# Performance work log

Hardware: AMD Instinct MI355X
Metric: run time of the kernel (lower is better)

## Reference

```python
import jax, jax.numpy as jnp
import numpy as np

DIM = 1024
HEADS = 16
DIM_HEAD = 64
DEPTH = 12
LN_EPS = 1e-5


def setup_inputs() -> dict:
    key = jax.random.key(0)
    k1, k2, k3 = jax.random.split(key, 3)
    B, N = 4, 2048
    inner = HEADS * DIM_HEAD
    x = jax.random.normal(k1, (B, N, DIM), dtype=jnp.float32)
    ln_w = jnp.ones((DIM,), jnp.float32)
    ln_b = jnp.zeros((DIM,), jnp.float32)
    w_qkv = jax.random.normal(k2, (DIM, 3 * inner), jnp.float32) * (DIM ** -0.5)
    w_out = jax.random.normal(k3, (inner, DIM), jnp.float32) * (inner ** -0.5)
    b_out = jnp.zeros((DIM,), jnp.float32)
    return {"x": x, "ln_w": ln_w, "ln_b": ln_b, "w_qkv": w_qkv,
            "w_out": w_out, "b_out": b_out, "layer_index": 2}


def reference(x, ln_w, ln_b, w_qkv, w_out, b_out, layer_index):
    B, N, D = x.shape
    scale = DIM_HEAD ** -0.5
    # LayerNorm
    mu = jnp.mean(x, axis=-1, keepdims=True)
    var = jnp.mean(jnp.square(x - mu), axis=-1, keepdims=True)
    xn = (x - mu) * jax.lax.rsqrt(var + LN_EPS) * ln_w + ln_b
    # QKV projection (no bias), split heads: b n (h d) -> b h n d
    qkv = xn @ w_qkv  # [B, N, 3*H*Dh]
    q, k, v = jnp.split(qkv, 3, axis=-1)
    def heads(t):
        return t.reshape(B, N, HEADS, DIM_HEAD).transpose(0, 2, 1, 3)
    q, k, v = heads(q), heads(k), heads(v)
    dots = jnp.einsum('bhnd,bhmd->bhnm', q, k) * scale  # [B,H,N,N]
    if layer_index < DEPTH // 2:
        attn = jax.nn.relu(dots)
    else:
        attn = jax.nn.softmax(dots, axis=-1)
    attn = attn / N  # divide by x.shape[1]
    out = jnp.einsum('bhnm,bhmd->bhnd', attn, v)
    out = out.transpose(0, 2, 1, 3).reshape(B, N, HEADS * DIM_HEAD)
    # to_out (heads > 1): Linear + (inactive) dropout
    return out @ w_out + b_out
```

## Files before the change

kernel.cpp:

```cpp
#include <hip/hip_runtime.h>
#include <stdint.h>

typedef __bf16 bf16x8 __attribute__((ext_vector_type(8)));
typedef __bf16 bf16x4 __attribute__((ext_vector_type(4)));
typedef float f32x4 __attribute__((ext_vector_type(4)));
typedef float f32x16 __attribute__((ext_vector_type(16)));

#define PSCALE (0.125f / 2048.0f)

#define GLOAD16(src, dst)                                                      \
  __builtin_amdgcn_global_load_lds(                                            \
      (__attribute__((address_space(1))) void*)const_cast<__bf16*>(src),       \
      (__attribute__((address_space(3))) void*)(dst), 16, 0, 0)

__global__ __launch_bounds__(256) void prep(
    const float* __restrict__ x, const float* __restrict__ lw,
    const float* __restrict__ lb, __bf16* __restrict__ xn,
    const float* __restrict__ w_qkv, __bf16* __restrict__ Wt1,
    const float* __restrict__ w_out, __bf16* __restrict__ Wt2) {
  __shared__ __bf16 T[64][72];
  __shared__ float red[8];
  const int b = blockIdx.x;
  const int t = threadIdx.x;
  if (b < 8192) {
    const float4 v = ((const float4*)(x + (size_t)b * 1024))[t];
    float s = v.x + v.y + v.z + v.w;
    float ss = v.x * v.x + v.y * v.y + v.z * v.z + v.w * v.w;
#pragma unroll
    for (int o = 32; o; o >>= 1) {
      s += __shfl_down(s, o);
      ss += __shfl_down(ss, o);
    }
    if ((t & 63) == 0) {
      red[t >> 6] = s;
      red[4 + (t >> 6)] = ss;
    }
    __syncthreads();
    const float tot = red[0] + red[1] + red[2] + red[3];
    const float tot2 = red[4] + red[5] + red[6] + red[7];
    const float mu = tot * (1.0f / 1024.0f);
    const float var = tot2 * (1.0f / 1024.0f) - mu * mu;
    const float rs = rsqrtf(var + 1e-5f);
    const float4 wv = ((const float4*)lw)[t];
    const float4 bv = ((const float4*)lb)[t];
    bf16x4 o;
    o[0] = (__bf16)((v.x - mu) * rs * wv.x + bv.x);
    o[1] = (__bf16)((v.y - mu) * rs * wv.y + bv.y);
    o[2] = (__bf16)((v.z - mu) * rs * wv.z + bv.z);
    o[3] = (__bf16)((v.w - mu) * rs * wv.w + bv.w);
    ((bf16x4*)xn)[(size_t)b * 256 + t] = o;
    return;
  }
  const float* A;
  __bf16* At;
  int R, C, bx, by;
  if (b < 8960) {
    const int ti = b - 8192;
    A = w_qkv; At = Wt1; R = 1024; C = 3072;
    bx = ti % 48; by = ti / 48;
  } else {
    const int ti = b - 8960;
    A = w_out; At = Wt2; R = 1024; C = 1024;
    bx = ti % 16; by = ti / 16;
  }
  const int rb = by * 64, cb = bx * 64;
  const int r = t >> 2, cg = t & 3;
#pragma unroll
  for (int k = 0; k < 4; ++k) {
    const float4 v =
        *(const float4*)(A + (size_t)(rb + r) * C + cb + cg * 16 + k * 4);
    T[cg * 16 + k * 4 + 0][r] = (__bf16)v.x;
    T[cg * 16 + k * 4 + 1][r] = (__bf16)v.y;
    T[cg * 16 + k * 4 + 2][r] = (__bf16)v.z;
    T[cg * 16 + k * 4 + 3][r] = (__bf16)v.w;
  }
  __syncthreads();
#pragma unroll
  for (int i = 0; i < 2; ++i) {
    const int j = i * 256 + t;
    const int c = j >> 3, s8 = j & 7;
    const bf16x8 o = *(const bf16x8*)&T[c][s8 * 8];
    *(bf16x8*)(At + (size_t)(cb + c) * R + rb + s8 * 8) = o;
  }
}

template <int MODE>
__global__ __launch_bounds__(512) void gemm_nt(
    const __bf16* __restrict__ A, const __bf16* __restrict__ B, int K,
    float* __restrict__ outF, __bf16* __restrict__ Qo, __bf16* __restrict__ Ko,
    __bf16* __restrict__ Vto, const float* __restrict__ bias) {
  __shared__ __bf16 Sm[3 * 24576];
  const int tid = threadIdx.x;
  const int lane = tid & 63, w = tid >> 6;
  const int g = lane >> 4, c15 = lane & 15;
  const int wr = w >> 2, wc = w & 3;
  const int linear = blockIdx.y * gridDim.x + blockIdx.x;
  const int per = (gridDim.x * gridDim.y) >> 3;
  const int nl = (linear & 7) * per + (linear >> 3);
  const int rb = (nl / gridDim.x) * 128, cb = (nl % gridDim.x) * 256;

  const __bf16* aSp[2];
  const __bf16* bSp[4];
  int aDo[2], bDo[4];
#pragma unroll
  for (int i = 0; i < 2; ++i) {
    const int j = i * 512 + tid, row = j >> 3, slot = j & 7;
    aSp[i] = A + (size_t)(rb + row) * K + ((slot ^ (row & 7)) << 3);
    aDo[i] = i * 4096 + w * 512;
  }
#pragma unroll
  for (int i = 0; i < 4; ++i) {
    const int j = i * 512 + tid, col = j >> 3, slot = j & 7;
    bSp[i] = B + (size_t)(cb + col) * K + ((slot ^ (col & 7)) << 3);
    bDo[i] = 8192 + i * 4096 + w * 512;
  }

  f32x4 acc[4][4] = {};
  const int nkb = K >> 6;

#pragma unroll
  for (int t = 0; t < 2; ++t) {
    __bf16* dst = Sm + t * 24576;
#pragma unroll
    for (int i = 0; i < 2; ++i) GLOAD16(aSp[i] + t * 64, dst + aDo[i]);
#pragma unroll
    for (int i = 0; i < 4; ++i) GLOAD16(bSp[i] + t * 64, dst + bDo[i]);
  }

  int cur = 0, stg = 2, koff = 128;
  for (int kb = 0; kb < nkb; ++kb) {
    if (kb == nkb - 1) {
      asm volatile("s_waitcnt vmcnt(0)" ::: "memory");
    } else {
      asm volatile("s_waitcnt vmcnt(6)" ::: "memory");
    }
    __builtin_amdgcn_s_barrier();
    const bool do_stage = (kb < nkb - 2);
    __bf16* sdst = Sm + stg * 24576;
    if (do_stage) {
#pragma unroll
      for (int i = 0; i < 2; ++i) GLOAD16(aSp[i] + koff, sdst + aDo[i]);
    }
    const __bf16* __restrict__ Ac = Sm + cur * 24576;
    const __bf16* __restrict__ Bc = Ac + 8192;
    {
      bf16x8 af[4], bfr[4];
      const int kc = g;
#pragma unroll
      for (int rt = 0; rt < 4; ++rt) {
        const int lr = wr * 64 + rt * 16 + c15;
        af[rt] = *(const bf16x8*)(Ac + lr * 64 + ((kc ^ (lr & 7)) << 3));
      }
#pragma unroll
      for (int ct = 0; ct < 4; ++ct) {
        const int lc = wc * 64 + ct * 16 + c15;
        bfr[ct] = *(const bf16x8*)(Bc + lc * 64 + ((kc ^ (lc & 7)) << 3));
      }
      __builtin_amdgcn_s_setprio(1);
#pragma unroll
      for (int rt = 0; rt < 4; ++rt)
#pragma unroll
        for (int ct = 0; ct < 4; ++ct)
          acc[rt][ct] = __builtin_amdgcn_mfma_f32_16x16x32_bf16(
              af[rt], bfr[ct], acc[rt][ct], 0, 0, 0);
      __builtin_amdgcn_s_setprio(0);
    }
    if (do_stage) {
#pragma unroll
      for (int i = 0; i < 4; ++i) GLOAD16(bSp[i] + koff, sdst + bDo[i]);
      koff += 64;
    }
    {
      bf16x8 af[4], bfr[4];
      const int kc = 4 + g;
#pragma unroll
      for (int rt = 0; rt < 4; ++rt) {
        const int lr = wr * 64 + rt * 16 + c15;
        af[rt] = *(const bf16x8*)(Ac + lr * 64 + ((kc ^ (lr & 7)) << 3));
      }
#pragma unroll
      for (int ct = 0; ct < 4; ++ct) {
        const int lc = wc * 64 + ct * 16 + c15;
        bfr[ct] = *(const bf16x8*)(Bc + lc * 64 + ((kc ^ (lc & 7)) << 3));
      }
      __builtin_amdgcn_s_setprio(1);
#pragma unroll
      for (int rt = 0; rt < 4; ++rt)
#pragma unroll
        for (int ct = 0; ct < 4; ++ct)
          acc[rt][ct] = __builtin_amdgcn_mfma_f32_16x16x32_bf16(
              af[rt], bfr[ct], acc[rt][ct], 0, 0, 0);
      __builtin_amdgcn_s_setprio(0);
    }
    cur = (cur == 2) ? 0 : cur + 1;
    stg = (stg == 2) ? 0 : stg + 1;
  }
  const int r00 = rb + wr * 64 + g * 4;
  if (MODE == 1) {
#pragma unroll
    for (int ct = 0; ct < 4; ++ct) {
      const int col = cb + wc * 64 + ct * 16 + c15;
      const float bv = bias[col];
#pragma unroll
      for (int rt = 0; rt < 4; ++rt) {
        const int row = r00 + rt * 16;
#pragma unroll
        for (int r = 0; r < 4; ++r)
          outF[(size_t)(row + r) * 1024 + col] = acc[rt][ct][r] + bv;
      }
    }
  } else {
#pragma unroll
    for (int ct = 0; ct < 4; ++ct) {
      const int col = cb + wc * 64 + ct * 16 + c15;
      const int part = col >> 10, rem = col & 1023;
      const int h = rem >> 6, d = rem & 63;
#pragma unroll
      for (int rt = 0; rt < 4; ++rt) {
        const int row = r00 + rt * 16;
        const int bi = row >> 11, n = row & 2047;
        const size_t bh = (size_t)bi * 16 + h;
        if (part == 2) {
          bf16x4 pv;
#pragma unroll
          for (int r = 0; r < 4; ++r) pv[r] = (__bf16)acc[rt][ct][r];
          *(bf16x4*)(Vto + (bh * 64 + d) * 2048 + n) = pv;
        } else if (part == 0) {
          __bf16* dst = Qo + (bh * 2048 + n) * 64 + d;
#pragma unroll
          for (int r = 0; r < 4; ++r)
            dst[(size_t)r * 64] = (__bf16)(acc[rt][ct][r] * PSCALE);
        } else {
          __bf16* dst = Ko + (bh * 2048 + n) * 64 + d;
#pragma unroll
          for (int r = 0; r < 4; ++r) dst[(size_t)r * 64] = (__bf16)acc[rt][ct][r];
        }
      }
    }
  }
}

__global__ __launch_bounds__(512, 4) void attn_relu(
    const __bf16* __restrict__ Q, const __bf16* __restrict__ K,
    const __bf16* __restrict__ Vt, __bf16* __restrict__ O) {
  __shared__ __bf16 Ks[2][128 * 64];
  __shared__ __bf16 Vs[2][64 * 128];
  const int tid = threadIdx.x;
  const int lane = tid & 63, wv = tid >> 6;
  const int hi = lane >> 5, c31 = lane & 31;
  const int bh = blockIdx.x, qb = blockIdx.y;
  const __bf16* Qg = Q + ((size_t)bh * 2048 + qb * 256) * 64;
  const __bf16* Kg = K + (size_t)bh * 2048 * 64;
  const __bf16* Vg = Vt + (size_t)bh * 64 * 2048;

  const __bf16* kp0;
  const __bf16* kp1;
  const __bf16* vp0;
  const __bf16* vp1;
  {
    const int j0 = tid, j1 = 512 + tid;
    const int X0 = j0 >> 3, s0 = j0 & 7;
    const int X1 = j1 >> 3, s1 = j1 & 7;
    const int K0 = (X0 & ~12) | ((X0 & 4) << 1) | ((X0 & 8) >> 1);
    const int K1 = (X1 & ~12) | ((X1 & 4) << 1) | ((X1 & 8) >> 1);
    kp0 = Kg + (size_t)K0 * 64 + ((s0 ^ (X0 & 7)) << 3);
    kp1 = Kg + (size_t)K1 * 64 + ((s1 ^ (X1 & 7)) << 3);
    const int d0_ = j0 >> 4, t0_ = j0 & 15;
    const int d1_ = j1 >> 4, t1_ = j1 & 15;
    vp0 = Vg + (size_t)d0_ * 2048 + ((t0_ ^ (d0_ & 15)) << 3);
    vp1 = Vg + (size_t)d1_ * 2048 + ((t1_ ^ (d1_ & 15)) << 3);
  }
  const int dstoff = wv * 64 * 8;

  bf16x8 qf[4];
#pragma unroll
  for (int dw = 0; dw < 4; ++dw)
    qf[dw] = *(const bf16x8*)(Qg + (wv * 32 + c31) * 64 + dw * 16 + hi * 8);
  f32x16 oacc[2] = {};

  GLOAD16(kp0, Ks[0] + dstoff);
  GLOAD16(kp1, Ks[0] + 512 * 8 + dstoff);
  GLOAD16(vp0, Vs[0] + dstoff);
  GLOAD16(vp1, Vs[0] + 512 * 8 + dstoff);
  kp0 += 128 * 64; kp1 += 128 * 64; vp0 += 128; vp1 += 128;

  for (int kb = 0; kb < 16; ++kb) {
    const int cur = kb & 1;
    if (kb < 15) {
      GLOAD16(kp0, Ks[cur ^ 1] + dstoff);
      GLOAD16(kp1, Ks[cur ^ 1] + 512 * 8 + dstoff);
      GLOAD16(vp0, Vs[cur ^ 1] + dstoff);
      GLOAD16(vp1, Vs[cur ^ 1] + 512 * 8 + dstoff);
      kp0 += 128 * 64; kp1 += 128 * 64; vp0 += 128; vp1 += 128;
      asm volatile("s_waitcnt vmcnt(4)" ::: "memory");
    } else {
      asm volatile("s_waitcnt vmcnt(0)" ::: "memory");
    }
    __builtin_amdgcn_s_barrier();
    const __bf16* __restrict__ Kc = Ks[cur];
    const __bf16* __restrict__ Vc = Vs[cur];
#pragma unroll
    for (int kb32 = 0; kb32 < 4; ++kb32) {
      bf16x8 kf[4];
      const int R = kb32 * 32 + c31;
#pragma unroll
      for (int dw = 0; dw < 4; ++dw)
        kf[dw] =
            *(const bf16x8*)(Kc + R * 64 + (((2 * dw + hi) ^ (R & 7)) << 3));
      f32x16 s = {};
      __builtin_amdgcn_s_setprio(1);
#pragma unroll
      for (int dw = 0; dw < 4; ++dw)
        s = __builtin_amdgcn_mfma_f32_32x32x16_bf16(kf[dw], qf[dw], s, 0, 0, 0);
      __builtin_amdgcn_s_setprio(0);
      bf16x8 pa[2];
#pragma unroll
      for (int wl = 0; wl < 2; ++wl)
#pragma unroll
        for (int e = 0; e < 8; ++e)
          pa[wl][e] = (__bf16)fmaxf(s[8 * wl + e], 0.0f);
      __builtin_amdgcn_s_setprio(1);
#pragma unroll
      for (int wl = 0; wl < 2; ++wl) {
        const int win = 2 * kb32 + wl;
#pragma unroll
        for (int dc = 0; dc < 2; ++dc) {
          const int d = dc * 32 + c31;
          const bf16x8 vb = *(const bf16x8*)(
              Vc + d * 128 + (((2 * win + hi) ^ (d & 15)) << 3));
          oacc[dc] = __builtin_amdgcn_mfma_f32_32x32x16_bf16(pa[wl], vb,
                                                             oacc[dc], 0, 0, 0);
        }
      }
      __builtin_amdgcn_s_setprio(0);
    }
    __builtin_amdgcn_s_barrier();
  }
  const int bi = bh >> 4, h = bh & 15;
#pragma unroll
  for (int dc = 0; dc < 2; ++dc) {
    const int col = h * 64 + dc * 32 + c31;
#pragma unroll
    for (int r = 0; r < 16; ++r) {
      const int q = wv * 32 + (r & 3) + 8 * (r >> 2) + 4 * hi;
      const int n0 = qb * 256 + q;
      O[((size_t)bi * 2048 + n0) * 1024 + col] = (__bf16)oacc[dc][r];
    }
  }
}

extern "C" void kernel_launch(void* const* d_in, const int* in_sizes, int n_in,
                              void* d_out, int out_size, void* d_ws,
                              size_t ws_size, hipStream_t stream) {
  (void)in_sizes; (void)n_in; (void)out_size; (void)ws_size;
  const float* x = (const float*)d_in[0];
  const float* ln_w = (const float*)d_in[1];
  const float* ln_b = (const float*)d_in[2];
  const float* w_qkv = (const float*)d_in[3];
  const float* w_out = (const float*)d_in[4];
  const float* b_out = (const float*)d_in[5];
  char* ws = (char*)d_ws;
  __bf16* xn = (__bf16*)(ws);
  __bf16* Wt1 = (__bf16*)(ws + (size_t)(16u << 20));
  __bf16* Wt2 = (__bf16*)(ws + (size_t)(22u << 20));
  __bf16* Qb = (__bf16*)(ws + (size_t)(24u << 20));
  __bf16* Kb = (__bf16*)(ws + (size_t)(40u << 20));
  __bf16* Vtb = (__bf16*)(ws + (size_t)(56u << 20));
  __bf16* Ob = (__bf16*)(ws + (size_t)(72u << 20));
  float* out = (float*)d_out;

  prep<<<9216, 256, 0, stream>>>(x, ln_w, ln_b, xn, w_qkv, Wt1, w_out, Wt2);
  gemm_nt<0><<<dim3(12, 64), 512, 0, stream>>>(xn, Wt1, 1024, nullptr, Qb, Kb,
                                               Vtb, nullptr);
  attn_relu<<<dim3(64, 8), 512, 0, stream>>>(Qb, Kb, Vtb, Ob);
  gemm_nt<1><<<dim3(4, 64), 512, 0, stream>>>(Ob, Wt2, 1024, out, nullptr,
                                              nullptr, nullptr, b_out);
}
```

Measured before the change: 161.0 us.

## Halve attention block threads, each wave computes two 32-row query groups

The ReLU attention kernel now runs 256 threads (4 waves) per block instead of 512. Each wave handles 64 query rows as two 32-row MFMA groups, so every K and V fragment read from LDS is reused for twice as many MFMAs. Each thread issues 4 K and 4 V async loads per tile, and the wait count is adjusted to match. The cost is more accumulator and Q registers per wave and fewer waves per block to hide latency.

```diff
diff --git a/kernel.cpp b/kernel.cpp
--- a/kernel.cpp
+++ b/kernel.cpp
@@ -240,7 +240,7 @@
   }
 }
 
-__global__ __launch_bounds__(512, 4) void attn_relu(
+__global__ __launch_bounds__(256, 2) void attn_relu(
     const __bf16* __restrict__ Q, const __bf16* __restrict__ K,
     const __bf16* __restrict__ Vt, __bf16* __restrict__ O) {
   __shared__ __bf16 Ks[2][128 * 64];
@@ -253,46 +253,45 @@
   const __bf16* Kg = K + (size_t)bh * 2048 * 64;
   const __bf16* Vg = Vt + (size_t)bh * 64 * 2048;
 
-  const __bf16* kp0;
-  const __bf16* kp1;
-  const __bf16* vp0;
-  const __bf16* vp1;
-  {
-    const int j0 = tid, j1 = 512 + tid;
-    const int X0 = j0 >> 3, s0 = j0 & 7;
-    const int X1 = j1 >> 3, s1 = j1 & 7;
-    const int K0 = (X0 & ~12) | ((X0 & 4) << 1) | ((X0 & 8) >> 1);
-    const int K1 = (X1 & ~12) | ((X1 & 4) << 1) | ((X1 & 8) >> 1);
-    kp0 = Kg + (size_t)K0 * 64 + ((s0 ^ (X0 & 7)) << 3);
-    kp1 = Kg + (size_t)K1 * 64 + ((s1 ^ (X1 & 7)) << 3);
-    const int d0_ = j0 >> 4, t0_ = j0 & 15;
-    const int d1_ = j1 >> 4, t1_ = j1 & 15;
-    vp0 = Vg + (size_t)d0_ * 2048 + ((t0_ ^ (d0_ & 15)) << 3);
-    vp1 = Vg + (size_t)d1_ * 2048 + ((t1_ ^ (d1_ & 15)) << 3);
-  }
-  const int dstoff = wv * 64 * 8;
-
-  bf16x8 qf[4];
-#pragma unroll
-  for (int dw = 0; dw < 4; ++dw)
-    qf[dw] = *(const bf16x8*)(Qg + (wv * 32 + c31) * 64 + dw * 16 + hi * 8);
-  f32x16 oacc[2] = {};
-
-  GLOAD16(kp0, Ks[0] + dstoff);
-  GLOAD16(kp1, Ks[0] + 512 * 8 + dstoff);
-  GLOAD16(vp0, Vs[0] + dstoff);
-  GLOAD16(vp1, Vs[0] + 512 * 8 + dstoff);
-  kp0 += 128 * 64; kp1 += 128 * 64; vp0 += 128; vp1 += 128;
+  const __bf16* kp[4];
+  const __bf16* vp[4];
+#pragma unroll
+  for (int i = 0; i < 4; ++i) {
+    const int j = i * 256 + tid;
+    const int X = j >> 3, s = j & 7;
+    const int KX = (X & ~12) | ((X & 4) << 1) | ((X & 8) >> 1);
+    kp[i] = Kg + (size_t)KX * 64 + ((s ^ (X & 7)) << 3);
+    const int d = j >> 4, sl = j & 15;
+    vp[i] = Vg + (size_t)d * 2048 + ((sl ^ (d & 15)) << 3);
+  }
+  const int dstoff = wv * 512;
+
+  bf16x8 qf[2][4];
+#pragma unroll
+  for (int qg = 0; qg < 2; ++qg)
+#pragma unroll
+    for (int dw = 0; dw < 4; ++dw)
+      qf[qg][dw] = *(const bf16x8*)(Qg + (wv * 64 + qg * 32 + c31) * 64 +
+                                    dw * 16 + hi * 8);
+  f32x16 oacc[2][2] = {};
+
+#pragma unroll
+  for (int i = 0; i < 4; ++i) GLOAD16(kp[i], Ks[0] + i * 2048 + dstoff);
+#pragma unroll
+  for (int i = 0; i < 4; ++i) GLOAD16(vp[i], Vs[0] + i * 2048 + dstoff);
 
   for (int kb = 0; kb < 16; ++kb) {
     const int cur = kb & 1;
     if (kb < 15) {
-      GLOAD16(kp0, Ks[cur ^ 1] + dstoff);
-      GLOAD16(kp1, Ks[cur ^ 1] + 512 * 8 + dstoff);
-      GLOAD16(vp0, Vs[cur ^ 1] + dstoff);
-      GLOAD16(vp1, Vs[cur ^ 1] + 512 * 8 + dstoff);
-      kp0 += 128 * 64; kp1 += 128 * 64; vp0 += 128; vp1 += 128;
-      asm volatile("s_waitcnt vmcnt(4)" ::: "memory");
+      const int nxt = cur ^ 1;
+      const int ko = (kb + 1) * 8192, vo = (kb + 1) * 128;
+#pragma unroll
+      for (int i = 0; i < 4; ++i)
+        GLOAD16(kp[i] + ko, Ks[nxt] + i * 2048 + dstoff);
+#pragma unroll
+      for (int i = 0; i < 4; ++i)
+        GLOAD16(vp[i] + vo, Vs[nxt] + i * 2048 + dstoff);
+      asm volatile("s_waitcnt vmcnt(8)" ::: "memory");
     } else {
       asm volatile("s_waitcnt vmcnt(0)" ::: "memory");
     }
@@ -307,18 +306,23 @@
       for (int dw = 0; dw < 4; ++dw)
         kf[dw] =
             *(const bf16x8*)(Kc + R * 64 + (((2 * dw + hi) ^ (R & 7)) << 3));
-      f32x16 s = {};
+      f32x16 s[2] = {{}, {}};
       __builtin_amdgcn_s_setprio(1);
 #pragma unroll
       for (int dw = 0; dw < 4; ++dw)
-        s = __builtin_amdgcn_mfma_f32_32x32x16_bf16(kf[dw], qf[dw], s, 0, 0, 0);
+#pragma unroll
+        for (int qg = 0; qg < 2; ++qg)
+          s[qg] = __builtin_amdgcn_mfma_f32_32x32x16_bf16(kf[dw], qf[qg][dw],
+                                                          s[qg], 0, 0, 0);
       __builtin_amdgcn_s_setprio(0);
-      bf16x8 pa[2];
-#pragma unroll
-      for (int wl = 0; wl < 2; ++wl)
-#pragma unroll
-        for (int e = 0; e < 8; ++e)
-          pa[wl][e] = (__bf16)fmaxf(s[8 * wl + e], 0.0f);
+      bf16x8 pa[2][2];
+#pragma unroll
+      for (int qg = 0; qg < 2; ++qg)
+#pragma unroll
+        for (int wl = 0; wl < 2; ++wl)
+#pragma unroll
+          for (int e = 0; e < 8; ++e)
+            pa[qg][wl][e] = (__bf16)fmaxf(s[qg][8 * wl + e], 0.0f);
       __builtin_amdgcn_s_setprio(1);
 #pragma unroll
       for (int wl = 0; wl < 2; ++wl) {
@@ -328,8 +332,10 @@
           const int d = dc * 32 + c31;
           const bf16x8 vb = *(const bf16x8*)(
               Vc + d * 128 + (((2 * win + hi) ^ (d & 15)) << 3));
-          oacc[dc] = __builtin_amdgcn_mfma_f32_32x32x16_bf16(pa[wl], vb,
-                                                             oacc[dc], 0, 0, 0);
+#pragma unroll
+          for (int qg = 0; qg < 2; ++qg)
+            oacc[qg][dc] = __builtin_amdgcn_mfma_f32_32x32x16_bf16(
+                pa[qg][wl], vb, oacc[qg][dc], 0, 0, 0);
         }
       }
       __builtin_amdgcn_s_setprio(0);
@@ -338,15 +344,17 @@
   }
   const int bi = bh >> 4, h = bh & 15;
 #pragma unroll
-  for (int dc = 0; dc < 2; ++dc) {
-    const int col = h * 64 + dc * 32 + c31;
-#pragma unroll
-    for (int r = 0; r < 16; ++r) {
-      const int q = wv * 32 + (r & 3) + 8 * (r >> 2) + 4 * hi;
-      const int n0 = qb * 256 + q;
-      O[((size_t)bi * 2048 + n0) * 1024 + col] = (__bf16)oacc[dc][r];
-    }
-  }
+  for (int qg = 0; qg < 2; ++qg)
+#pragma unroll
+    for (int dc = 0; dc < 2; ++dc) {
+      const int col = h * 64 + dc * 32 + c31;
+#pragma unroll
+      for (int r = 0; r < 16; ++r) {
+        const int q = wv * 64 + qg * 32 + (r & 3) + 8 * (r >> 2) + 4 * hi;
+        const int n0 = qb * 256 + q;
+        O[((size_t)bi * 2048 + n0) * 1024 + col] = (__bf16)oacc[qg][dc][r];
+      }
+    }
 }
 
 extern "C" void kernel_launch(void* const* d_in, const int* in_sizes, int n_in,
@@ -372,7 +380,7 @@
   prep<<<9216, 256, 0, stream>>>(x, ln_w, ln_b, xn, w_qkv, Wt1, w_out, Wt2);
   gemm_nt<0><<<dim3(12, 64), 512, 0, stream>>>(xn, Wt1, 1024, nullptr, Qb, Kb,
                                                Vtb, nullptr);
-  attn_relu<<<dim3(64, 8), 512, 0, stream>>>(Qb, Kb, Vtb, Ob);
+  attn_relu<<<dim3(64, 8), 256, 0, stream>>>(Qb, Kb, Vtb, Ob);
   gemm_nt<1><<<dim3(4, 64), 512, 0, stream>>>(Ob, Wt2, 1024, out, nullptr,
                                               nullptr, nullptr, b_out);
 }
```

Measured after the change: 169.4 us (median of 2 runs). 5.3% more time.

## Read V fragments directly from global memory instead of staging through LDS

Applied to the files above, without the earlier changes.

Removes the double-buffered V tile from shared memory in the relu attention kernel and has each wave load its V operand fragments straight from global memory, leaving only K staged via async global-to-LDS copies. This halves the kernel's LDS footprint, which may allow more resident blocks, and removes the V LDS writes and reads. In exchange, all eight waves redundantly fetch the same V data through the cache hierarchy, and global-load latency now sits inside the inner MFMA loop.

```diff
diff --git a/kernel.cpp b/kernel.cpp
--- a/kernel.cpp
+++ b/kernel.cpp
@@ -244,7 +244,6 @@
     const __bf16* __restrict__ Q, const __bf16* __restrict__ K,
     const __bf16* __restrict__ Vt, __bf16* __restrict__ O) {
   __shared__ __bf16 Ks[2][128 * 64];
-  __shared__ __bf16 Vs[2][64 * 128];
   const int tid = threadIdx.x;
   const int lane = tid & 63, wv = tid >> 6;
   const int hi = lane >> 5, c31 = lane & 31;
@@ -253,24 +252,15 @@
   const __bf16* Kg = K + (size_t)bh * 2048 * 64;
   const __bf16* Vg = Vt + (size_t)bh * 64 * 2048;
 
-  const __bf16* kp0;
-  const __bf16* kp1;
-  const __bf16* vp0;
-  const __bf16* vp1;
-  {
-    const int j0 = tid, j1 = 512 + tid;
-    const int X0 = j0 >> 3, s0 = j0 & 7;
-    const int X1 = j1 >> 3, s1 = j1 & 7;
-    const int K0 = (X0 & ~12) | ((X0 & 4) << 1) | ((X0 & 8) >> 1);
-    const int K1 = (X1 & ~12) | ((X1 & 4) << 1) | ((X1 & 8) >> 1);
-    kp0 = Kg + (size_t)K0 * 64 + ((s0 ^ (X0 & 7)) << 3);
-    kp1 = Kg + (size_t)K1 * 64 + ((s1 ^ (X1 & 7)) << 3);
-    const int d0_ = j0 >> 4, t0_ = j0 & 15;
-    const int d1_ = j1 >> 4, t1_ = j1 & 15;
-    vp0 = Vg + (size_t)d0_ * 2048 + ((t0_ ^ (d0_ & 15)) << 3);
-    vp1 = Vg + (size_t)d1_ * 2048 + ((t1_ ^ (d1_ & 15)) << 3);
-  }
-  const int dstoff = wv * 64 * 8;
+  const __bf16* kp[2];
+#pragma unroll
+  for (int i = 0; i < 2; ++i) {
+    const int j = i * 512 + tid;
+    const int X = j >> 3, s = j & 7;
+    const int KX = (X & ~12) | ((X & 4) << 1) | ((X & 8) >> 1);
+    kp[i] = Kg + (size_t)KX * 64 + ((s ^ (X & 7)) << 3);
+  }
+  const int dstoff = wv * 512;
 
   bf16x8 qf[4];
 #pragma unroll
@@ -278,27 +268,23 @@
     qf[dw] = *(const bf16x8*)(Qg + (wv * 32 + c31) * 64 + dw * 16 + hi * 8);
   f32x16 oacc[2] = {};
 
-  GLOAD16(kp0, Ks[0] + dstoff);
-  GLOAD16(kp1, Ks[0] + 512 * 8 + dstoff);
-  GLOAD16(vp0, Vs[0] + dstoff);
-  GLOAD16(vp1, Vs[0] + 512 * 8 + dstoff);
-  kp0 += 128 * 64; kp1 += 128 * 64; vp0 += 128; vp1 += 128;
+#pragma unroll
+  for (int i = 0; i < 2; ++i) GLOAD16(kp[i], Ks[0] + i * 4096 + dstoff);
 
   for (int kb = 0; kb < 16; ++kb) {
     const int cur = kb & 1;
     if (kb < 15) {
-      GLOAD16(kp0, Ks[cur ^ 1] + dstoff);
-      GLOAD16(kp1, Ks[cur ^ 1] + 512 * 8 + dstoff);
-      GLOAD16(vp0, Vs[cur ^ 1] + dstoff);
-      GLOAD16(vp1, Vs[cur ^ 1] + 512 * 8 + dstoff);
-      kp0 += 128 * 64; kp1 += 128 * 64; vp0 += 128; vp1 += 128;
-      asm volatile("s_waitcnt vmcnt(4)" ::: "memory");
+      const int ko = (kb + 1) * 8192;
+#pragma unroll
+      for (int i = 0; i < 2; ++i)
+        GLOAD16(kp[i] + ko, Ks[cur ^ 1] + i * 4096 + dstoff);
+      asm volatile("s_waitcnt vmcnt(2)" ::: "memory");
     } else {
       asm volatile("s_waitcnt vmcnt(0)" ::: "memory");
     }
     __builtin_amdgcn_s_barrier();
     const __bf16* __restrict__ Kc = Ks[cur];
-    const __bf16* __restrict__ Vc = Vs[cur];
+    const __bf16* __restrict__ Vb = Vg + kb * 128;
 #pragma unroll
     for (int kb32 = 0; kb32 < 4; ++kb32) {
       bf16x8 kf[4];
@@ -319,19 +305,22 @@
 #pragma unroll
         for (int e = 0; e < 8; ++e)
           pa[wl][e] = (__bf16)fmaxf(s[8 * wl + e], 0.0f);
+      bf16x8 vb[2][2];
+#pragma unroll
+      for (int wl = 0; wl < 2; ++wl) {
+        const int kofs = (2 * kb32 + wl) * 16 + hi * 8;
+#pragma unroll
+        for (int dc = 0; dc < 2; ++dc)
+          vb[wl][dc] = *(const bf16x8*)(
+              Vb + (size_t)(dc * 32 + c31) * 2048 + kofs);
+      }
       __builtin_amdgcn_s_setprio(1);
 #pragma unroll
-      for (int wl = 0; wl < 2; ++wl) {
-        const int win = 2 * kb32 + wl;
-#pragma unroll
-        for (int dc = 0; dc < 2; ++dc) {
-          const int d = dc * 32 + c31;
-          const bf16x8 vb = *(const bf16x8*)(
-              Vc + d * 128 + (((2 * win + hi) ^ (d & 15)) << 3));
-          oacc[dc] = __builtin_amdgcn_mfma_f32_32x32x16_bf16(pa[wl], vb,
-                                                             oacc[dc], 0, 0, 0);
-        }
-      }
+      for (int wl = 0; wl < 2; ++wl)
+#pragma unroll
+        for (int dc = 0; dc < 2; ++dc)
+          oacc[dc] = __builtin_amdgcn_mfma_f32_32x32x16_bf16(
+              pa[wl], vb[wl][dc], oacc[dc], 0, 0, 0);
       __builtin_amdgcn_s_setprio(0);
     }
     __builtin_amdgcn_s_barrier();
```

After: 232.9 us. 1.45x slower.
